# Optimization experiments

Hardware: AMD Instinct MI355X
Metric: run time of the kernel (lower is better)

The kernel has to match this reference:

```python
import jax, jax.numpy as jnp
import numpy as np

N_MSB = 4
WB = 8       # weight bits
ABNM = 8     # activation bits for non-MVM ops
NL = 0.1     # noise level
B, IN, H = 256, 1024, 1024


def pact_a(x, a):
    # sign(x) * 0.5 * (|x| - ||x|-a| + a)  == sign(x)*min(|x|, a) for a>0
    return jnp.sign(x) * 0.5 * (jnp.abs(x) - jnp.abs(jnp.abs(x) - a) + a)


def _quant_val(x, bits, x_range):
    step = 2.0 ** (bits - 1)
    x01 = jnp.clip(x / x_range, -1.0 + 1.0 / step, 1.0 - 1.0 / step)
    return jnp.round(x01 * step) / step * x_range


def quant_ste(x, bits, x_range):
    # QuantFunc: straight-through estimator (identity grad wrt x, none wrt range)
    return x + jax.lax.stop_gradient(_quant_val(x, bits, x_range) - x)


def bitsplit(x, n_msb):
    # x in [0,1] -> n_msb binary planes stacked on axis 0, plus beta coefficients
    l1 = 2.0 ** n_msb - 1.0
    ys, betas = [], []
    for i in range(n_msb):
        l2 = 2.0 ** (n_msb - (i + 1))
        betas.append(l2 / l1)
        ys.append(jnp.mod(jnp.floor(jnp.round(l1 * x) / l2), 2.0))
    return jnp.stack(ys), jnp.asarray(betas, dtype=x.dtype)


def noisy_qmm(x, w, b, eps_w, eps_b):
    # CustomMM_bmm: quantized weights + gaussian noise in fwd; STE-style bwd.
    w_eff = w + jax.lax.stop_gradient(_quant_val(w, WB, 1.0) - w + eps_w * jnp.max(w) * NL)
    b_eff = b + jax.lax.stop_gradient(_quant_val(b, WB, 1.0) - b + eps_b * jnp.max(b) * NL)
    return jnp.einsum('nbi,nio->nbo', x, w_eff) + b_eff  # [n_msb, B, 4H]


def lstm_cell_q_bs(input, hx, cx, weight_ih, weight_hh, bias_ih, bias_hh,
                   eps_w_ih, eps_w_hh, eps_b_ih, eps_b_hh,
                   a1, a3, a4, a5, a6, a7, a8, a9, a10, a11):
    inp01 = (pact_a(input, a1) + a1) / (a1 * 2.0)            # [B, IN] in [0,1]
    inp_msb, beta = bitsplit(inp01, N_MSB)                   # [n_msb,B,IN], [n_msb]
    o1 = noisy_qmm(inp_msb, weight_ih, bias_ih, eps_w_ih, eps_b_ih)
    o2 = noisy_qmm(inp_msb, weight_hh, bias_hh, eps_w_hh, eps_b_hh)
    out = (o1 > 0.5).astype(inp01.dtype) + (o2 > 0.5).astype(inp01.dtype)
    gates = jnp.einsum('n,nbo->bo', beta, out)               # part1; part2 undefined in source -> 0
    i, j, f, o = jnp.split(gates, 4, axis=1)                 # each [B, H]
    forget_gate_out = quant_ste(pact_a(jax.nn.sigmoid(f), a3), ABNM, a3)
    input_gate_out = quant_ste(pact_a(jax.nn.sigmoid(i), a4), ABNM, a4)
    activation_out = quant_ste(pact_a(jnp.tanh(j), a5), ABNM, a5)
    output_gate_out = quant_ste(pact_a(jax.nn.sigmoid(o), a6), ABNM, a6)
    gated_cell = quant_ste(pact_a(cx * forget_gate_out, a7), ABNM, a7)
    activated_input = quant_ste(pact_a(input_gate_out * activation_out, a8), ABNM, a8)
    new_c = quant_ste(pact_a(gated_cell + activated_input, a9), ABNM, a9)
    activated_cell = quant_ste(pact_a(jnp.tanh(new_c), a10), ABNM, a10)
    new_h = quant_ste(pact_a(activated_cell * output_gate_out, a11), ABNM, a11)
    return new_h, new_c


def setup_inputs() -> dict:
    key = jax.random.key(0)
    ks = jax.random.split(key, 12)
    d = {
        'input': jax.random.normal(ks[0], (B, IN), jnp.float32),
        'hx': jax.random.normal(ks[1], (B, H), jnp.float32),
        'cx': jax.random.normal(ks[2], (B, H), jnp.float32),
        'weight_ih': jax.random.normal(ks[3], (N_MSB, IN, 4 * H), jnp.float32),
        'weight_hh': jax.random.normal(ks[4], (N_MSB, IN, 4 * H), jnp.float32),
        'bias_ih': jax.random.normal(ks[5], (N_MSB, 1, 4 * H), jnp.float32),
        'bias_hh': jax.random.normal(ks[6], (N_MSB, 1, 4 * H), jnp.float32),
        'eps_w_ih': jax.random.normal(ks[7], (N_MSB, IN, 4 * H), jnp.float32),
        'eps_w_hh': jax.random.normal(ks[8], (N_MSB, IN, 4 * H), jnp.float32),
        'eps_b_ih': jax.random.normal(ks[9], (N_MSB, 1, 4 * H), jnp.float32),
        'eps_b_hh': jax.random.normal(ks[10], (N_MSB, 1, 4 * H), jnp.float32),
    }
    a_init = {'a1': 128.0, 'a3': 1.0, 'a4': 1.0, 'a5': 1.0, 'a6': 1.0,
              'a7': 4.0, 'a8': 1.0, 'a9': 4.0, 'a10': 1.0, 'a11': 4.0}
    for name, v in a_init.items():
        d[name] = jnp.array([v], jnp.float32)
    return d


def reference(input, hx, cx, weight_ih, weight_hh, bias_ih, bias_hh,
              eps_w_ih, eps_w_hh, eps_b_ih, eps_b_hh,
              a1, a3, a4, a5, a6, a7, a8, a9, a10, a11):
    return lstm_cell_q_bs(input, hx, cx, weight_ih, weight_hh, bias_ih, bias_hh,
                          eps_w_ih, eps_w_hh, eps_b_ih, eps_b_hh,
                          a1, a3, a4, a5, a6, a7, a8, a9, a10, a11)
```

## Files before the change

### kernel.cpp

```cpp
#include <hip/hip_runtime.h>
#include <hip/hip_bf16.h>
#include <math.h>

typedef int   v4i __attribute__((ext_vector_type(4)));
typedef float v4f __attribute__((ext_vector_type(4)));

#define B_DIM   256
#define IN_DIM  1024
#define H4      4096
#define NPLANE  4
#define WELEM   (NPLANE * IN_DIM * H4)
#define XELEM   (B_DIM * IN_DIM)

#define WS_X_OFF      (64 + 262144)
#define WS_CMP_OFF    (64 + 262144 + 1048576)

__global__ void k_max(const float* __restrict__ wih, const float* __restrict__ whh,
                      const float* __restrict__ bih, const float* __restrict__ bhh,
                      float* __restrict__ outm) {
  int b = blockIdx.x, t = threadIdx.x;
  const float* src; long n4; int slot; long bb, nb;
  if (b < 512)       { src = wih; n4 = WELEM / 4; slot = 0; bb = b;       nb = 512; }
  else if (b < 1024) { src = whh; n4 = WELEM / 4; slot = 1; bb = b - 512; nb = 512; }
  else if (b == 1024){ src = bih; n4 = 16384 / 4; slot = 2; bb = 0;       nb = 1;   }
  else               { src = bhh; n4 = 16384 / 4; slot = 3; bb = 0;       nb = 1;   }
  const v4f* p = (const v4f*)src;
  float m = -3.4e38f;
  for (long i = bb * 256 + t; i < n4; i += nb * 256) {
    v4f v = p[i];
    m = fmaxf(m, fmaxf(fmaxf(v.x, v.y), fmaxf(v.z, v.w)));
  }
#pragma unroll
  for (int off = 32; off >= 1; off >>= 1) m = fmaxf(m, __shfl_down(m, off, 64));
  __shared__ float sm[4];
  int w = t >> 6, ln = t & 63;
  if (ln == 0) sm[w] = m;
  __syncthreads();
  if (t == 0) {
    m = fmaxf(fmaxf(sm[0], sm[1]), fmaxf(sm[2], sm[3]));
    atomicMax((int*)&outm[slot], __float_as_int(m));
  }
}

__global__ void k_prep(const float* __restrict__ input, const float* __restrict__ a1p,
                       signed char* __restrict__ X) {
  int gid = blockIdx.x * 256 + threadIdx.x;
  float a1 = a1p[0];
  float x = input[gid];
  float t = fabsf(x), u = fabsf(t - a1);
  float sg = (x > 0.f) ? 0.5f : ((x < 0.f) ? -0.5f : 0.f);
  float p = sg * ((t - u) + a1);
  float inp01 = (p + a1) / (a1 * 2.0f);
  float q = rintf(15.0f * inp01);
  int qi = (int)q;
#pragma unroll
  for (int pl = 0; pl < 4; ++pl)
    X[pl * XELEM + gid] = (signed char)((qi >> (3 - pl)) & 1);
}

__global__ __launch_bounds__(512, 2) void k_gemm(
    const float* __restrict__ Wih, const float* __restrict__ Whh,
    const float* __restrict__ Eih, const float* __restrict__ Ehh,
    const float* __restrict__ bih, const float* __restrict__ bhh,
    const float* __restrict__ ebih, const float* __restrict__ ebhh,
    const float* __restrict__ maxm,
    const signed char* __restrict__ X, unsigned char* __restrict__ cmp) {
  const int ntile = blockIdx.x;
  const int sp = blockIdx.y;
  const int s = sp >> 2, plane = sp & 3;
  const float* W = s ? Whh : Wih;
  const float* E = s ? Ehh : Eih;
  const float maxw = maxm[s];

  const int tid = threadIdx.x;
  const int wave = tid >> 6, lane = tid & 63, quad = lane >> 4, l15 = lane & 15;

  __shared__ __align__(16) unsigned char Blds[2 * 4 * 32 * 64];

  const int kl  = tid >> 3;
  const int nc4 = (tid & 7) << 2;
  const int p  = (lane >> 3) & 3;
  const int sq = p & 1, qq = p >> 1;
  const unsigned sel1 = sq ? 0x03070206u : 0x05010400u;
  const unsigned sel2 = qq ? 0x03020706u : 0x05040100u;
  const int snW = nc4 + 2 * sq + qq;
  const int kqW = (wave << 1) + (lane >> 5);
  const int wr_off = snW * 64 + ((((kqW >> 2) ^ ((snW >> 1) & 3)) << 4) | ((kqW & 3) << 2));

  v4i acc[4][2][2];
#pragma unroll
  for (int d = 0; d < 4; ++d)
#pragma unroll
    for (int m = 0; m < 2; ++m)
#pragma unroll
      for (int n = 0; n < 2; ++n) acc[d][m][n] = (v4i){0, 0, 0, 0};

  const size_t cstep = (size_t)64 * H4;
  const float* wp = W + ((size_t)plane * IN_DIM + kl) * H4 + (size_t)ntile * 32 + nc4;
  const float* ep = E + ((size_t)plane * IN_DIM + kl) * H4 + (size_t)ntile * 32 + nc4;

  const signed char* Xp = X + plane * XELEM;
  const int arow0 = wave * 32 + l15;

  auto digitize4 = [&](v4f w4, v4f e4, unsigned pk[4]) {
    pk[0] = pk[1] = pk[2] = pk[3] = 0;
#pragma unroll
    for (int j = 0; j < 4; ++j) {
      float w = w4[j], ev = e4[j];
      float xc = fminf(fmaxf(w, -0.9921875f), 0.9921875f);
      float qv = rintf(xc * 128.f) * 0.0078125f;
      float noise = (ev * maxw) * 0.1f;
      float a = w + ((qv - w) + noise);
      float x0 = a * 8.f;    float f0 = rintf(x0); float r0 = x0 - f0;
      float x1 = r0 * 128.f; float f1 = rintf(x1); float r1 = x1 - f1;
      float x2 = r1 * 128.f; float f2 = rintf(x2); float r2 = x2 - f2;
      float x3 = r2 * 128.f; float f3 = rintf(x3);
      pk[0] |= ((unsigned)((int)f0 & 255)) << (8 * j);
      pk[1] |= ((unsigned)((int)f1 & 255)) << (8 * j);
      pk[2] |= ((unsigned)((int)f2 & 255)) << (8 * j);
      pk[3] |= ((unsigned)((int)f3 & 255)) << (8 * j);
    }
  };
  auto transpose_write = [&](const unsigned pk[4], int bf) {
    unsigned char* base = Blds + bf * 8192 + wr_off;
#pragma unroll
    for (int d = 0; d < 4; ++d) {
      unsigned A = pk[d];
      unsigned t = (unsigned)__shfl_xor((int)A, 8, 64);
      unsigned D = __builtin_amdgcn_perm(t, A, sel1);
      unsigned Ex = (unsigned)__shfl_xor((int)D, 16, 64);
      unsigned o = __builtin_amdgcn_perm(Ex, D, sel2);
      *(unsigned*)(base + d * 2048) = o;
    }
  };

  unsigned pk[4];
  {
    v4f w4 = *(const v4f*)wp;
    v4f e4 = *(const v4f*)ep;
    digitize4(w4, e4, pk);
    transpose_write(pk, 0);
  }
  v4f wA = *(const v4f*)(wp + cstep);
  v4f eA = *(const v4f*)(ep + cstep);
  v4i afr[2];
  afr[0] = *(const v4i*)(Xp + (arow0) * IN_DIM + quad * 16);
  afr[1] = *(const v4i*)(Xp + (arow0 + 16) * IN_DIM + quad * 16);
  __syncthreads();

  for (int ch = 0; ch < 16; ++ch) {
    const int buf = ch & 1;
    v4f wB = wA, eB = eA;
    v4i anx0 = afr[0], anx1 = afr[1];
    if (ch < 14) {
      wB = *(const v4f*)(wp + (size_t)(ch + 2) * cstep);
      eB = *(const v4f*)(ep + (size_t)(ch + 2) * cstep);
    }
    if (ch < 15) {
      anx0 = *(const v4i*)(Xp + (arow0) * IN_DIM + (ch + 1) * 64 + quad * 16);
      anx1 = *(const v4i*)(Xp + (arow0 + 16) * IN_DIM + (ch + 1) * 64 + quad * 16);
    }
    const unsigned char* rb = Blds + buf * 8192;
#pragma unroll
    for (int d = 0; d < 4; ++d) {
#pragma unroll
      for (int ns = 0; ns < 2; ++ns) {
        const int nr = ns * 16 + l15;
        v4i bfr = *(const v4i*)(rb + d * 2048 + nr * 64 + ((quad ^ ((nr >> 1) & 3)) << 4));
        acc[d][0][ns] = __builtin_amdgcn_mfma_i32_16x16x64_i8(afr[0], bfr, acc[d][0][ns], 0, 0, 0);
        acc[d][1][ns] = __builtin_amdgcn_mfma_i32_16x16x64_i8(afr[1], bfr, acc[d][1][ns], 0, 0, 0);
      }
    }
    if (ch < 15) {
      digitize4(wA, eA, pk);
      transpose_write(pk, buf ^ 1);
      wA = wB; eA = eB;
    }
    afr[0] = anx0; afr[1] = anx1;
    __syncthreads();
  }

  const float* bp  = s ? bhh : bih;
  const float* ebp = s ? ebhh : ebih;
  const float mb = maxm[2 + s];
  const double inv = 1.0 / 16777216.0;
  unsigned char* cp = cmp + (size_t)sp * B_DIM * H4;
#pragma unroll
  for (int ns = 0; ns < 2; ++ns) {
    int col = ntile * 32 + ns * 16 + l15;
    float bv = bp[plane * H4 + col], ev = ebp[plane * H4 + col];
    float xc = fminf(fmaxf(bv, -0.9921875f), 0.9921875f);
    float qv = rintf(xc * 128.f) * 0.0078125f;
    float noise = (ev * mb) * 0.1f;
    float beff = bv + ((qv - bv) + noise);
    double th = 0.5 - (double)beff;
#pragma unroll
    for (int ms = 0; ms < 2; ++ms) {
#pragma unroll
      for (int r = 0; r < 4; ++r) {
        long long T = ((long long)acc[0][ms][ns][r] << 21) + ((long long)acc[1][ms][ns][r] << 14)
                    + ((long long)acc[2][ms][ns][r] << 7)  +  (long long)acc[3][ms][ns][r];
        int row = wave * 32 + ms * 16 + quad * 4 + r;
        cp[(size_t)row * H4 + col] = ((double)T * inv > th) ? 1 : 0;
      }
    }
  }
}

__device__ __forceinline__ float pact_(float x, float a) {
  float t = fabsf(x), u = fabsf(t - a);
  float sg = (x > 0.f) ? 0.5f : ((x < 0.f) ? -0.5f : 0.f);
  return sg * ((t - u) + a);
}
__device__ __forceinline__ float quant_(float x, float a) {
  float xr = x / a;
  xr = fminf(fmaxf(xr, -0.9921875f), 0.9921875f);
  return rintf(xr * 128.f) * 0.0078125f * a;
}
__device__ __forceinline__ float sigm_(float x) { return 1.0f / (1.0f + expf(-x)); }

__global__ void k_pointwise(const unsigned char* __restrict__ cmp, const float* __restrict__ cx,
                            const float* a3, const float* a4, const float* a5, const float* a6,
                            const float* a7, const float* a8, const float* a9, const float* a10,
                            const float* a11, float* __restrict__ out) {
  int idx = blockIdx.x * 256 + threadIdx.x;
  int b = idx >> 10, h = idx & 1023;
  float g[4];
#pragma unroll
  for (int gi = 0; gi < 4; ++gi) {
    int col = gi * 1024 + h;
    float acc = 0.f;
#pragma unroll
    for (int n = 0; n < 4; ++n) {
      int o = (int)cmp[((size_t)(0 * 4 + n) * B_DIM + b) * H4 + col]
            + (int)cmp[((size_t)(1 * 4 + n) * B_DIM + b) * H4 + col];
      float beta = (float)(8 >> n) / 15.0f;
      acc = acc + beta * (float)o;
    }
    g[gi] = acc;
  }
  float fg = quant_(pact_(sigm_(g[2]), a3[0]), a3[0]);
  float ig = quant_(pact_(sigm_(g[0]), a4[0]), a4[0]);
  float ac = quant_(pact_(tanhf(g[1]), a5[0]), a5[0]);
  float og = quant_(pact_(sigm_(g[3]), a6[0]), a6[0]);
  float cxv = cx[idx];
  float gc = quant_(pact_(cxv * fg, a7[0]), a7[0]);
  float ai = quant_(pact_(ig * ac, a8[0]), a8[0]);
  float nc = quant_(pact_(gc + ai, a9[0]), a9[0]);
  float acl = quant_(pact_(tanhf(nc), a10[0]), a10[0]);
  float nh = quant_(pact_(acl * og, a11[0]), a11[0]);
  out[idx] = nh;
  out[XELEM + idx] = nc;
}

extern "C" void kernel_launch(void* const* d_in, const int* in_sizes, int n_in,
                              void* d_out, int out_size, void* d_ws, size_t ws_size,
                              hipStream_t stream) {
  (void)in_sizes; (void)n_in; (void)out_size; (void)ws_size;
  const float* input = (const float*)d_in[0];
  const float* cx    = (const float*)d_in[2];
  const float* wih   = (const float*)d_in[3];
  const float* whh   = (const float*)d_in[4];
  const float* bih   = (const float*)d_in[5];
  const float* bhh   = (const float*)d_in[6];
  const float* ewih  = (const float*)d_in[7];
  const float* ewhh  = (const float*)d_in[8];
  const float* ebih  = (const float*)d_in[9];
  const float* ebhh  = (const float*)d_in[10];
  const float* a1    = (const float*)d_in[11];
  const float* a3    = (const float*)d_in[12];
  const float* a4    = (const float*)d_in[13];
  const float* a5    = (const float*)d_in[14];
  const float* a6    = (const float*)d_in[15];
  const float* a7    = (const float*)d_in[16];
  const float* a8    = (const float*)d_in[17];
  const float* a9    = (const float*)d_in[18];
  const float* a10   = (const float*)d_in[19];
  const float* a11   = (const float*)d_in[20];
  float* out = (float*)d_out;

  char* ws = (char*)d_ws;
  float*         maxm = (float*)ws;
  signed char*   X    = (signed char*)(ws + WS_X_OFF);
  unsigned char* cmp  = (unsigned char*)(ws + WS_CMP_OFF);

  hipMemsetAsync(ws, 0, 64, stream);
  k_max<<<1026, 256, 0, stream>>>(wih, whh, bih, bhh, maxm);
  k_prep<<<1024, 256, 0, stream>>>(input, a1, X);
  k_gemm<<<dim3(128, 8), 512, 0, stream>>>(wih, whh, ewih, ewhh, bih, bhh, ebih, ebhh,
                                           maxm, X, cmp);
  k_pointwise<<<1024, 256, 0, stream>>>(cmp, cx, a3, a4, a5, a6, a7, a8, a9, a10, a11, out);
}
```

Before: 341.6 us.

## Replace iterative weight digit split with offset fixed-point and row-sum correction

Weight digitization now converts each effective weight to one offset fixed-point integer and extracts 7-bit digits with shifts and byte permutes, instead of the chain of round/subtract/scale steps. Offsetting makes every digit non-negative, so a per-row popcount of the activation bit planes, gathered in the prep kernel with shuffle reductions and atomics, is subtracted in the epilogue to undo the offset. This cuts ALU work in the GEMM's digitize stage, which sits in the main loop's critical path. In exchange it adds atomics and a reduction to prep, and it relies on the rounding and digit ranges matching the old decomposition exactly.

Result: faster. 333.6 us (-2.4%).

```diff
diff --git a/kernel.cpp b/kernel.cpp
--- a/kernel.cpp
+++ b/kernel.cpp
@@ -12,6 +12,7 @@
 #define WELEM   (NPLANE * IN_DIM * H4)
 #define XELEM   (B_DIM * IN_DIM)
 
+#define WS_RS_OFF     64
 #define WS_X_OFF      (64 + 262144)
 #define WS_CMP_OFF    (64 + 262144 + 1048576)
 
@@ -43,8 +44,9 @@
 }
 
 __global__ void k_prep(const float* __restrict__ input, const float* __restrict__ a1p,
-                       signed char* __restrict__ X) {
-  int gid = blockIdx.x * 256 + threadIdx.x;
+                       signed char* __restrict__ X, int* __restrict__ rowsum) {
+  int tid = threadIdx.x;
+  int gid = blockIdx.x * 256 + tid;
   float a1 = a1p[0];
   float x = input[gid];
   float t = fabsf(x), u = fabsf(t - a1);
@@ -56,6 +58,23 @@
 #pragma unroll
   for (int pl = 0; pl < 4; ++pl)
     X[pl * XELEM + gid] = (signed char)((qi >> (3 - pl)) & 1);
+
+  int v = ((qi >> 3) & 1) | (((qi >> 2) & 1) << 8) | (((qi >> 1) & 1) << 16) | ((qi & 1) << 24);
+#pragma unroll
+  for (int off = 32; off >= 1; off >>= 1) v += __shfl_down(v, off, 64);
+  __shared__ int sv[4];
+  int wid = tid >> 6, ln = tid & 63;
+  if (ln == 0) sv[wid] = v;
+  __syncthreads();
+  if (tid == 0) {
+    int b = blockIdx.x >> 2;
+#pragma unroll
+    for (int pl = 0; pl < 4; ++pl) {
+      int cnt = ((sv[0] >> (8 * pl)) & 255) + ((sv[1] >> (8 * pl)) & 255)
+              + ((sv[2] >> (8 * pl)) & 255) + ((sv[3] >> (8 * pl)) & 255);
+      atomicAdd(&rowsum[pl * 256 + b], cnt);
+    }
+  }
 }
 
 __global__ __launch_bounds__(512, 2) void k_gemm(
@@ -63,7 +82,7 @@
     const float* __restrict__ Eih, const float* __restrict__ Ehh,
     const float* __restrict__ bih, const float* __restrict__ bhh,
     const float* __restrict__ ebih, const float* __restrict__ ebhh,
-    const float* __restrict__ maxm,
+    const float* __restrict__ maxm, const int* __restrict__ rowsum,
     const signed char* __restrict__ X, unsigned char* __restrict__ cmp) {
   const int ntile = blockIdx.x;
   const int sp = blockIdx.y;
@@ -103,7 +122,7 @@
   const int arow0 = wave * 32 + l15;
 
   auto digitize4 = [&](v4f w4, v4f e4, unsigned pk[4]) {
-    pk[0] = pk[1] = pk[2] = pk[3] = 0;
+    int mm[4];
 #pragma unroll
     for (int j = 0; j < 4; ++j) {
       float w = w4[j], ev = e4[j];
@@ -111,14 +130,18 @@
       float qv = rintf(xc * 128.f) * 0.0078125f;
       float noise = (ev * maxw) * 0.1f;
       float a = w + ((qv - w) + noise);
-      float x0 = a * 8.f;    float f0 = rintf(x0); float r0 = x0 - f0;
-      float x1 = r0 * 128.f; float f1 = rintf(x1); float r1 = x1 - f1;
-      float x2 = r1 * 128.f; float f2 = rintf(x2); float r2 = x2 - f2;
-      float x3 = r2 * 128.f; float f3 = rintf(x3);
-      pk[0] |= ((unsigned)((int)f0 & 255)) << (8 * j);
-      pk[1] |= ((unsigned)((int)f1 & 255)) << (8 * j);
-      pk[2] |= ((unsigned)((int)f2 & 255)) << (8 * j);
-      pk[3] |= ((unsigned)((int)f3 & 255)) << (8 * j);
+      mm[j] = (int)rintf(a * 16777216.0f) + (1 << 27);
+    }
+#pragma unroll
+    for (int d = 0; d < 4; ++d) {
+      const int sh = 21 - 7 * d;
+      unsigned a0 = (unsigned)(mm[0] >> sh);
+      unsigned a1 = (unsigned)(mm[1] >> sh);
+      unsigned a2 = (unsigned)(mm[2] >> sh);
+      unsigned a3 = (unsigned)(mm[3] >> sh);
+      unsigned t1 = __builtin_amdgcn_perm(a1, a0, 0x00000400u);
+      unsigned t2 = __builtin_amdgcn_perm(a3, a2, 0x00000400u);
+      pk[d] = __builtin_amdgcn_perm(t2, t1, 0x05040100u) & 0x7f7f7f7fu;
     }
   };
   auto transpose_write = [&](const unsigned pk[4], int bf) {
@@ -183,6 +206,7 @@
   const float* bp  = s ? bhh : bih;
   const float* ebp = s ? ebhh : ebih;
   const float mb = maxm[2 + s];
+  const int* rs = rowsum + plane * 256;
   const double inv = 1.0 / 16777216.0;
   unsigned char* cp = cmp + (size_t)sp * B_DIM * H4;
 #pragma unroll
@@ -198,9 +222,10 @@
     for (int ms = 0; ms < 2; ++ms) {
 #pragma unroll
       for (int r = 0; r < 4; ++r) {
+        int row = wave * 32 + ms * 16 + quad * 4 + r;
         long long T = ((long long)acc[0][ms][ns][r] << 21) + ((long long)acc[1][ms][ns][r] << 14)
-                    + ((long long)acc[2][ms][ns][r] << 7)  +  (long long)acc[3][ms][ns][r];
-        int row = wave * 32 + ms * 16 + quad * 4 + r;
+                    + ((long long)acc[2][ms][ns][r] << 7)  +  (long long)acc[3][ms][ns][r]
+                    - ((long long)rs[row] << 27);
         cp[(size_t)row * H4 + col] = ((double)T * inv > th) ? 1 : 0;
       }
     }
@@ -280,14 +305,15 @@
   float* out = (float*)d_out;
 
   char* ws = (char*)d_ws;
-  float*         maxm = (float*)ws;
-  signed char*   X    = (signed char*)(ws + WS_X_OFF);
-  unsigned char* cmp  = (unsigned char*)(ws + WS_CMP_OFF);
-
-  hipMemsetAsync(ws, 0, 64, stream);
+  float*         maxm   = (float*)ws;
+  int*           rowsum = (int*)(ws + WS_RS_OFF);
+  signed char*   X      = (signed char*)(ws + WS_X_OFF);
+  unsigned char* cmp    = (unsigned char*)(ws + WS_CMP_OFF);
+
+  hipMemsetAsync(ws, 0, 64 + 4096, stream);
   k_max<<<1026, 256, 0, stream>>>(wih, whh, bih, bhh, maxm);
-  k_prep<<<1024, 256, 0, stream>>>(input, a1, X);
+  k_prep<<<1024, 256, 0, stream>>>(input, a1, X, rowsum);
   k_gemm<<<dim3(128, 8), 512, 0, stream>>>(wih, whh, ewih, ewhh, bih, bhh, ebih, ebhh,
-                                           maxm, X, cmp);
+                                           maxm, rowsum, X, cmp);
   k_pointwise<<<1024, 256, 0, stream>>>(cmp, cx, a3, a4, a5, a6, a7, a8, a9, a10, a11, out);
 }
```
